# Optimization experiments

Measured on AMD Instinct MI355X. Metric: run time of the kernel, lower is better.

## Reference

```python
import jax, jax.numpy as jnp
import numpy as np


def setup_inputs() -> dict:
    key = jax.random.key(0)
    k1, k2 = jax.random.split(key)
    b, n, d = 8, 4096, 512
    num_codebooks, codebook_size = 1, 8192
    x = jax.random.normal(k1, (b, n, d), dtype=jnp.float32)
    embed = jax.random.normal(k2, (num_codebooks, codebook_size, d), dtype=jnp.float32)
    return {"x": x, "embed": embed}


def reference(x, embed):
    # Eval-mode forward of EuclideanCodebook (temperature 0 -> argmax of -cdist).
    # x: [b, n, d]; embed: [h, C, d] with h = num_codebooks = 1.
    b, n, d = x.shape
    h, C, _ = embed.shape
    flatten = x.reshape(h, b * n, d)                       # h * d packing (h=1)

    # dist = -cdist(flatten, embed): negative euclidean distance [h, N, C]
    x2 = jnp.sum(flatten * flatten, axis=-1, keepdims=True)   # [h, N, 1]
    e2 = jnp.sum(embed * embed, axis=-1)[:, None, :]          # [h, 1, C]
    xe = jnp.einsum('hnd,hcd->hnc', flatten, embed)           # [h, N, C]
    d2 = jnp.clip(x2 + e2 - 2.0 * xe, 0.0)
    dist = -jnp.sqrt(d2)                                      # [h, N, C]

    # gumbel_sample at temp 0 / eval -> straight argmax
    embed_ind_flat = jnp.argmax(dist, axis=-1)                # [h, N]

    # quantize = batched_embedding(embed_ind, embed): gather codes
    quantize = jnp.take_along_axis(embed, embed_ind_flat[..., None], axis=1)  # [h, N, d]

    # unpack + drop the codebook dim (needs_codebook_dim path)
    quantize = quantize.reshape(b, n, d)
    embed_ind = embed_ind_flat.reshape(b, n)
    dist = dist.reshape(h, b, n, C)  # dist keeps the codebook dim, as in source
    return quantize, embed_ind, dist
```

## Files before the change

kernel.cpp:

```cpp
#include <hip/hip_runtime.h>
#include <hip/hip_fp16.h>
#include <stdint.h>

typedef _Float16 f16x8 __attribute__((ext_vector_type(8)));
typedef _Float16 f16x4 __attribute__((ext_vector_type(4)));
typedef float    f32x4 __attribute__((ext_vector_type(4)));

static constexpr int NROWS = 32768;
static constexpr int NCODE = 8192;
static constexpr int DDIM  = 512;
static constexpr int BM = 256, BN = 256, BK = 64;
static constexpr int NBM = NROWS / BM;
static constexpr int NBN = NCODE / BN;
static constexpr int NPART = NBN * 2;

static constexpr size_t OFF_IND  = (size_t)NROWS * DDIM;
static constexpr size_t OFF_DIST = OFF_IND + NROWS;

static constexpr size_t WS_XH   = 0;
static constexpr size_t WS_XL   = WS_XH + (size_t)NROWS * DDIM * 2;
static constexpr size_t WS_EH   = WS_XL + (size_t)NROWS * DDIM * 2;
static constexpr size_t WS_EL   = WS_EH + (size_t)NCODE * DDIM * 2;
static constexpr size_t WS_X2   = WS_EL + (size_t)NCODE * DDIM * 2;
static constexpr size_t WS_E2   = WS_X2 + (size_t)NROWS * 4;
static constexpr size_t WS_PART = WS_E2 + (size_t)NCODE * 4;

__device__ inline void gload_lds16(const void* g, void* l) {
  __builtin_amdgcn_global_load_lds((const __attribute__((address_space(1))) void*)g,
                                   (__attribute__((address_space(3))) void*)l,
                                   16, 0, 0);
}

__global__ __launch_bounds__(128)
void prep_kernel(const float* __restrict__ x, const float* __restrict__ e,
                 _Float16* __restrict__ xh, _Float16* __restrict__ xl,
                 _Float16* __restrict__ eh, _Float16* __restrict__ el,
                 float* __restrict__ x2, float* __restrict__ e2)
{
  int bid = blockIdx.x;
  const float* src; _Float16 *dh, *dl; float* nrm;
  if (bid < NROWS) {
    src = x + (size_t)bid * DDIM;
    dh = xh + (size_t)bid * DDIM;  dl = xl + (size_t)bid * DDIM;
    nrm = x2 + bid;
  } else {
    int r = bid - NROWS;
    src = e + (size_t)r * DDIM;
    dh = eh + (size_t)r * DDIM;    dl = el + (size_t)r * DDIM;
    nrm = e2 + r;
  }
  int t = threadIdx.x;
  float4 v = reinterpret_cast<const float4*>(src)[t];
  double s = (double)v.x*v.x + (double)v.y*v.y + (double)v.z*v.z + (double)v.w*v.w;
  f16x4 h, l;
  h.x = (_Float16)v.x; l.x = (_Float16)(v.x - (float)h.x);
  h.y = (_Float16)v.y; l.y = (_Float16)(v.y - (float)h.y);
  h.z = (_Float16)v.z; l.z = (_Float16)(v.z - (float)h.z);
  h.w = (_Float16)v.w; l.w = (_Float16)(v.w - (float)h.w);
  reinterpret_cast<f16x4*>(dh)[t] = h;
  reinterpret_cast<f16x4*>(dl)[t] = l;
  #pragma unroll
  for (int m = 1; m < 64; m <<= 1) s += __shfl_xor(s, m);
  __shared__ double sh[2];
  if ((t & 63) == 0) sh[t >> 6] = s;
  __syncthreads();
  if (t == 0) nrm[0] = (float)(sh[0] + sh[1]);
}

#define BARx __builtin_amdgcn_s_barrier()
#define VMC(n)  asm volatile("s_waitcnt vmcnt(" #n ")" ::: "memory")

__device__ __forceinline__ void MMX(f32x4 (&ac)[2][4], const f16x8 (&af)[2][2],
                                    const f16x8 (&bf)[4][2]) {
  __builtin_amdgcn_s_setprio(1);
  #pragma unroll
  for (int m = 0; m < 2; ++m)
    #pragma unroll
    for (int n = 0; n < 4; ++n)
      #pragma unroll
      for (int ks = 0; ks < 2; ++ks)
        ac[m][n] = __builtin_amdgcn_mfma_f32_16x16x32_f16(af[m][ks], bf[n][ks], ac[m][n], 0, 0, 0);
  __builtin_amdgcn_s_setprio(0);
}

__global__ __launch_bounds__(512, 1)
void dist_gemm_kernel(const _Float16* __restrict__ xh, const _Float16* __restrict__ xl,
                      const _Float16* __restrict__ eh, const _Float16* __restrict__ el,
                      const float* __restrict__ x2, const float* __restrict__ e2,
                      float* __restrict__ dist, float2* __restrict__ part)
{
  __shared__ _Float16 L[2][2][BM * BK];

  const int tid  = threadIdx.x;
  const int wid  = tid >> 6;
  const int lane = tid & 63;
  const int qwr  = wid >> 1;
  const int qwc  = wid & 1;

  const int flat = blockIdx.x;
  const int xcd  = flat & 7;
  const int idx  = flat >> 3;
  const int bn   = xcd * 4 + (idx & 3);
  const int bm   = idx >> 2;
  const int R  = bm * BM;
  const int Cc = bn * BN;

  const int l3 = lane >> 3;
  const int l7 = lane & 7;
  const int srcslot = ((l7 ^ l3) << 4);

  auto STAGE_HALF = [&](int t, int nb, int half) {
    const int ab = half & 1;
    const int hh = half >> 1;
    const _Float16* base;
    size_t rowbase;
    if (ab == 0) { base = (t < 16) ? xh : xl;              rowbase = (size_t)R;  }
    else         { base = (t < 8 || t >= 16) ? eh : el;    rowbase = (size_t)Cc; }
    const int k0b = (t & 7) * (BK * 2);
    #pragma unroll
    for (int i = 0; i < 2; ++i) {
      const int rr = hh * 128 + wid * 16 + i * 8;
      gload_lds16((const char*)base + (rowbase + rr + l3) * (DDIM * 2) + k0b + srcslot,
                  &L[nb][ab][rr * BK]);
    }
  };

  const int l15   = lane & 15;
  const int kslot = (lane >> 4) << 4;

  auto LDA = [&](f16x8 (&af)[2][2], int b, int mq) {
    #pragma unroll
    for (int m = 0; m < 2; ++m)
      #pragma unroll
      for (int ks = 0; ks < 2; ++ks) {
        const int row = mq * 128 + qwr * 32 + m * 16 + l15;
        const int kb  = (ks * 64 + kslot) ^ ((row & 7) << 4);
        af[m][ks] = *(const f16x8*)((const char*)&L[b][0][0] + row * 128 + kb);
      }
  };
  auto LDB = [&](f16x8 (&bf)[4][2], int b, int nq) {
    #pragma unroll
    for (int n = 0; n < 4; ++n)
      #pragma unroll
      for (int ks = 0; ks < 2; ++ks) {
        const int row = nq * 128 + qwc * 64 + n * 16 + l15;
        const int kb  = (ks * 64 + kslot) ^ ((row & 7) << 4);
        bf[n][ks] = *(const f16x8*)((const char*)&L[b][1][0] + row * 128 + kb);
      }
  };

  f32x4 acc[2][2][2][4] = {};

  STAGE_HALF(0, 0, 0);
  STAGE_HALF(0, 0, 1);
  STAGE_HALF(0, 0, 2);
  STAGE_HALF(0, 0, 3);

  for (int t = 0; t < 23; ++t) {
    const int b = t & 1;
    f16x8 af0[2][2], af1[2][2], bf0[4][2], bf1[4][2];

    STAGE_HALF(t + 1, b ^ 1, 0);
    STAGE_HALF(t + 1, b ^ 1, 1);
    VMC(6);  BARx;
    LDA(af0, b, 0);
    LDB(bf0, b, 0);
    LDA(af1, b, 1);
    MMX(acc[0][0], af0, bf0);
    MMX(acc[1][0], af1, bf0);

    STAGE_HALF(t + 1, b ^ 1, 2);
    STAGE_HALF(t + 1, b ^ 1, 3);
    VMC(8);  BARx;
    LDB(bf1, b, 1);
    MMX(acc[1][1], af1, bf1);
    MMX(acc[0][1], af0, bf1);
  }

  {
    f16x8 af0[2][2], af1[2][2], bf0[4][2], bf1[4][2];
    VMC(2);  BARx;
    LDA(af0, 1, 0);
    LDB(bf0, 1, 0);
    LDA(af1, 1, 1);
    MMX(acc[0][0], af0, bf0);
    MMX(acc[1][0], af1, bf0);
    VMC(0);  BARx;
    LDB(bf1, 1, 1);
    MMX(acc[1][1], af1, bf1);
    MMX(acc[0][1], af0, bf1);
  }

  const int q    = lane >> 4;
  const int csub = lane & 15;

  float e2v[2][4];
  #pragma unroll
  for (int nq = 0; nq < 2; ++nq)
    #pragma unroll
    for (int n = 0; n < 4; ++n)
      e2v[nq][n] = e2[Cc + nq * 128 + qwc * 64 + n * 16 + csub];

  float bestv[16], besti[16];
  int rix = 0;
  #pragma unroll
  for (int mq = 0; mq < 2; ++mq)
    #pragma unroll
    for (int m = 0; m < 2; ++m)
      #pragma unroll
      for (int j = 0; j < 4; ++j, ++rix) {
        const int row = R + mq * 128 + qwr * 32 + m * 16 + q * 4 + j;
        const float xv = x2[row];
        float* drow = dist + (size_t)row * NCODE;
        float bv = -3.0e38f, bi = 0.0f;
        #pragma unroll
        for (int nq = 0; nq < 2; ++nq)
          #pragma unroll
          for (int n = 0; n < 4; ++n) {
            const int col = Cc + nq * 128 + qwc * 64 + n * 16 + csub;
            float xe = acc[mq][nq][m][n][j];
            float d2 = fmaxf((xv + e2v[nq][n]) - 2.0f * xe, 0.0f);
            float dv = -sqrtf(d2);
            drow[col] = dv;
            if (dv > bv) { bv = dv; bi = (float)col; }
          }
        bestv[rix] = bv;
        besti[rix] = bi;
      }

  #pragma unroll
  for (int msk = 1; msk < 16; msk <<= 1) {
    #pragma unroll
    for (int r = 0; r < 16; ++r) {
      float ov = __shfl_xor(bestv[r], msk);
      float oi = __shfl_xor(besti[r], msk);
      if (ov > bestv[r] || (ov == bestv[r] && oi < besti[r])) { bestv[r] = ov; besti[r] = oi; }
    }
  }
  if (csub == 0) {
    int rr = 0;
    #pragma unroll
    for (int mq = 0; mq < 2; ++mq)
      #pragma unroll
      for (int m = 0; m < 2; ++m)
        #pragma unroll
        for (int j = 0; j < 4; ++j, ++rr) {
          const int row = R + mq * 128 + qwr * 32 + m * 16 + q * 4 + j;
          part[(size_t)row * NPART + bn * 2 + qwc] = make_float2(bestv[rr], besti[rr]);
        }
  }
}

__global__ __launch_bounds__(64)
void reduce_gather_kernel(const float2* __restrict__ part, const float* __restrict__ embed,
                          float* __restrict__ quant, float* __restrict__ ind)
{
  const int row = blockIdx.x;
  const int l = threadIdx.x;
  float2 a = part[(size_t)row * NPART + l];
  float bv = a.x, bi = a.y;
  #pragma unroll
  for (int m = 1; m < 64; m <<= 1) {
    float ov = __shfl_xor(bv, m);
    float oi = __shfl_xor(bi, m);
    if (ov > bv || (ov == bv && oi < bi)) { bv = ov; bi = oi; }
  }
  if (l == 0) ind[row] = bi;
  const int idx = (int)bi;
  const float4* src = reinterpret_cast<const float4*>(embed + (size_t)idx * DDIM);
  float4* dst = reinterpret_cast<float4*>(quant + (size_t)row * DDIM);
  dst[l]      = src[l];
  dst[l + 64] = src[l + 64];
}

extern "C" void kernel_launch(void* const* d_in, const int* in_sizes, int n_in,
                              void* d_out, int out_size, void* d_ws, size_t ws_size,
                              hipStream_t stream) {
  const float* x     = (const float*)d_in[0];
  const float* embed = (const float*)d_in[1];

  char* ws = (char*)d_ws;
  _Float16* xh = (_Float16*)(ws + WS_XH);
  _Float16* xl = (_Float16*)(ws + WS_XL);
  _Float16* eh = (_Float16*)(ws + WS_EH);
  _Float16* el = (_Float16*)(ws + WS_EL);
  float*    x2 = (float*)(ws + WS_X2);
  float*    e2 = (float*)(ws + WS_E2);
  float2*   part = (float2*)(ws + WS_PART);

  float* quant = (float*)d_out;
  float* ind   = (float*)d_out + OFF_IND;
  float* dist  = (float*)d_out + OFF_DIST;

  prep_kernel<<<dim3(NROWS + NCODE), 128, 0, stream>>>(x, embed, xh, xl, eh, el, x2, e2);
  dist_gemm_kernel<<<dim3(NBM * NBN), 512, 0, stream>>>(xh, xl, eh, el, x2, e2, dist, part);
  reduce_gather_kernel<<<dim3(NROWS), 64, 0, stream>>>(part, embed, quant, ind);
}
```

Measured before the change: 956.0 us.

## Load codebook operand directly from global into registers, bypassing LDS

The B (codebook) tile is no longer staged through shared memory; each wave reads its B fragments straight from global memory, and only the A tile stays double-buffered in LDS. This halves LDS use and removes LDS reads and writes for B. In exchange, B fragments are re-fetched by every wave row from L2, raising global traffic and exposing load latency next to the MFMA work.

```diff
diff --git a/kernel.cpp b/kernel.cpp
--- a/kernel.cpp
+++ b/kernel.cpp
@@ -89,7 +89,7 @@
                       const float* __restrict__ x2, const float* __restrict__ e2,
                       float* __restrict__ dist, float2* __restrict__ part)
 {
-  __shared__ _Float16 L[2][2][BM * BK];
+  __shared__ _Float16 L[2][BM * BK];
 
   const int tid  = threadIdx.x;
   const int wid  = tid >> 6;
@@ -109,19 +109,14 @@
   const int l7 = lane & 7;
   const int srcslot = ((l7 ^ l3) << 4);
 
-  auto STAGE_HALF = [&](int t, int nb, int half) {
-    const int ab = half & 1;
-    const int hh = half >> 1;
-    const _Float16* base;
-    size_t rowbase;
-    if (ab == 0) { base = (t < 16) ? xh : xl;              rowbase = (size_t)R;  }
-    else         { base = (t < 8 || t >= 16) ? eh : el;    rowbase = (size_t)Cc; }
+  auto STAGE_A = [&](int t, int nb, int hh) {
+    const _Float16* base = (t < 16) ? xh : xl;
     const int k0b = (t & 7) * (BK * 2);
     #pragma unroll
     for (int i = 0; i < 2; ++i) {
       const int rr = hh * 128 + wid * 16 + i * 8;
-      gload_lds16((const char*)base + (rowbase + rr + l3) * (DDIM * 2) + k0b + srcslot,
-                  &L[nb][ab][rr * BK]);
+      gload_lds16((const char*)base + (size_t)(R + rr + l3) * (DDIM * 2) + k0b + srcslot,
+                  &L[nb][rr * BK]);
     }
   };
 
@@ -135,58 +130,55 @@
       for (int ks = 0; ks < 2; ++ks) {
         const int row = mq * 128 + qwr * 32 + m * 16 + l15;
         const int kb  = (ks * 64 + kslot) ^ ((row & 7) << 4);
-        af[m][ks] = *(const f16x8*)((const char*)&L[b][0][0] + row * 128 + kb);
+        af[m][ks] = *(const f16x8*)((const char*)&L[b][0] + row * 128 + kb);
       }
   };
-  auto LDB = [&](f16x8 (&bf)[4][2], int b, int nq) {
+
+  auto LDB_G = [&](f16x8 (&bf)[4][2], int t, int nq) {
+    const char* base = (const char*)((t < 8 || t >= 16) ? eh : el);
+    const char* bp = base + (size_t)(Cc + nq * 128 + qwc * 64 + l15) * (DDIM * 2)
+                          + (t & 7) * (BK * 2) + kslot;
     #pragma unroll
     for (int n = 0; n < 4; ++n)
       #pragma unroll
-      for (int ks = 0; ks < 2; ++ks) {
-        const int row = nq * 128 + qwc * 64 + n * 16 + l15;
-        const int kb  = (ks * 64 + kslot) ^ ((row & 7) << 4);
-        bf[n][ks] = *(const f16x8*)((const char*)&L[b][1][0] + row * 128 + kb);
-      }
+      for (int ks = 0; ks < 2; ++ks)
+        bf[n][ks] = *(const f16x8*)(bp + n * 16 * (DDIM * 2) + ks * 64);
   };
 
   f32x4 acc[2][2][2][4] = {};
 
-  STAGE_HALF(0, 0, 0);
-  STAGE_HALF(0, 0, 1);
-  STAGE_HALF(0, 0, 2);
-  STAGE_HALF(0, 0, 3);
+  STAGE_A(0, 0, 0);
+  STAGE_A(0, 0, 1);
 
   for (int t = 0; t < 23; ++t) {
     const int b = t & 1;
     f16x8 af0[2][2], af1[2][2], bf0[4][2], bf1[4][2];
 
-    STAGE_HALF(t + 1, b ^ 1, 0);
-    STAGE_HALF(t + 1, b ^ 1, 1);
-    VMC(6);  BARx;
+    LDB_G(bf0, t, 0);
+    STAGE_A(t + 1, b ^ 1, 0);
+    VMC(2);  BARx;
     LDA(af0, b, 0);
-    LDB(bf0, b, 0);
     LDA(af1, b, 1);
     MMX(acc[0][0], af0, bf0);
     MMX(acc[1][0], af1, bf0);
 
-    STAGE_HALF(t + 1, b ^ 1, 2);
-    STAGE_HALF(t + 1, b ^ 1, 3);
-    VMC(8);  BARx;
-    LDB(bf1, b, 1);
+    LDB_G(bf1, t, 1);
+    STAGE_A(t + 1, b ^ 1, 1);
+    VMC(2);  BARx;
     MMX(acc[1][1], af1, bf1);
     MMX(acc[0][1], af0, bf1);
   }
 
   {
     f16x8 af0[2][2], af1[2][2], bf0[4][2], bf1[4][2];
-    VMC(2);  BARx;
+    LDB_G(bf0, 23, 0);
+    VMC(0);  BARx;
     LDA(af0, 1, 0);
-    LDB(bf0, 1, 0);
     LDA(af1, 1, 1);
     MMX(acc[0][0], af0, bf0);
     MMX(acc[1][0], af1, bf0);
-    VMC(0);  BARx;
-    LDB(bf1, 1, 1);
+    LDB_G(bf1, 23, 1);
+    VMC(0);
     MMX(acc[1][1], af1, bf1);
     MMX(acc[0][1], af0, bf1);
   }
```

Result: slower. 2.158 ms (+125.7%).
